# Kernel tuning notes

Hardware: AMD Instinct MI355X
Metric: run time of the kernel (lower is better)

Reference implementation:

```python
import jax, jax.numpy as jnp
import numpy as np

N_NODES = 100000
N_EDGES = 1600000
IN_F = 512
OUT_F = 128


def setup_inputs() -> dict:
    key = jax.random.key(0)
    k1, k2, k3, k4, k5 = jax.random.split(key, 5)
    x = jax.random.normal(k1, (N_NODES, IN_F), dtype=jnp.float32)
    adj_row = jnp.sort(jax.random.randint(k2, (N_EDGES,), 0, N_NODES, dtype=jnp.int32))
    adj_col = jax.random.randint(k3, (N_EDGES,), 0, N_NODES, dtype=jnp.int32)
    adj_vals = jax.random.uniform(k4, (N_EDGES,), dtype=jnp.float32)
    # Xavier-uniform init like nn.init.xavier_uniform_
    limit = float(np.sqrt(6.0 / (IN_F + OUT_F)))
    weight = jax.random.uniform(k5, (IN_F, OUT_F), minval=-limit, maxval=limit, dtype=jnp.float32)
    return {"x": x, "adj_row": adj_row, "adj_col": adj_col, "adj_vals": adj_vals, "weight": weight}


def reference(x, adj_row, adj_col, adj_vals, weight):
    # support = input @ weight  (dense GEMM; torch.spmm with dense-equivalent input)
    support = x @ weight                      # [N, OUT_F]
    # output = adj @ support, adj in COO: gather cols, scale, segment-sum by row
    msgs = adj_vals[:, None] * support[adj_col]          # [E, OUT_F]
    output = jax.ops.segment_sum(msgs, adj_row, num_segments=N_NODES)  # [N, OUT_F]
    return output
```

## Files before the change

### kernel.cpp

```cpp
#include <hip/hip_runtime.h>
#include <hip/hip_bf16.h>

typedef __bf16 bf16;
typedef __attribute__((ext_vector_type(8))) __bf16 bf16x8;
typedef __attribute__((ext_vector_type(4))) __bf16 bf16x4;
typedef __attribute__((ext_vector_type(2))) __bf16 bf16x2;
typedef __attribute__((ext_vector_type(4))) float f32x4;

#define IN_F 512
#define OUT_F 128
#define BM 64
#define BK 64
#define NKT (IN_F / BK)
#define CHUNK 128
#define UNR 16

__global__ __launch_bounds__(256) void wt_convert_kernel(const float* __restrict__ w,
                                                         bf16* __restrict__ wt) {
    int idx = blockIdx.x * 256 + threadIdx.x;
    int n = idx >> 9;
    int k = idx & 511;
    wt[idx] = (bf16)w[k * OUT_F + n];
}

__global__ __launch_bounds__(256) void gemm_kernel(const float* __restrict__ x,
                                                   const bf16* __restrict__ wt,
                                                   bf16* __restrict__ support,
                                                   int n_nodes) {
    __shared__ bf16 As[2][BM * BK];
    __shared__ bf16 Bs[2][OUT_F * BK];

    const int tid  = threadIdx.x;
    const int lane = tid & 63;
    const int wid  = tid >> 6;
    const int row0 = blockIdx.x * BM;

    float4 av[4];
    bf16x8 bv[4];

    auto load_tile = [&](int kt) {
        const int k0 = kt * BK;
        #pragma unroll
        for (int i = 0; i < 4; ++i) {
            int li = i * 256 + tid;
            int r = li >> 4, c4 = li & 15;
            int grow = row0 + r;
            float4 v = {0.f, 0.f, 0.f, 0.f};
            if (grow < n_nodes)
                v = *reinterpret_cast<const float4*>(x + (size_t)grow * IN_F + k0 + c4 * 4);
            av[i] = v;
        }
        #pragma unroll
        for (int i = 0; i < 4; ++i) {
            int li = i * 256 + tid;
            int r = li >> 3, c8 = li & 7;
            bv[i] = *reinterpret_cast<const bf16x8*>(wt + (size_t)r * IN_F + k0 + c8 * 8);
        }
    };

    auto write_tile = [&](int buf) {
        char* Ab = (char*)As[buf];
        char* Bb = (char*)Bs[buf];
        #pragma unroll
        for (int i = 0; i < 4; ++i) {
            int li = i * 256 + tid;
            int r = li >> 4, c4 = li & 15;
            bf16x4 b;
            b[0] = (bf16)av[i].x; b[1] = (bf16)av[i].y;
            b[2] = (bf16)av[i].z; b[3] = (bf16)av[i].w;
            *reinterpret_cast<bf16x4*>(Ab + ((r * 128 + c4 * 8) ^ ((r & 7) << 4))) = b;
        }
        #pragma unroll
        for (int i = 0; i < 4; ++i) {
            int li = i * 256 + tid;
            int r = li >> 3, c8 = li & 7;
            *reinterpret_cast<bf16x8*>(Bb + ((r * 128 + c8 * 16) ^ ((r & 7) << 4))) = bv[i];
        }
    };

    f32x4 acc[4][2] = {};

    load_tile(0);
    write_tile(0);
    __syncthreads();

    for (int kt = 0; kt < NKT; ++kt) {
        const int cur = kt & 1;
        if (kt < NKT - 1) load_tile(kt + 1);

        const char* Ab = (const char*)As[cur];
        const char* Bb = (const char*)Bs[cur];
        #pragma unroll
        for (int kk = 0; kk < 2; ++kk) {
            const int kbyte = kk * 64 + (lane >> 4) * 16;
            bf16x8 a[4], b[2];
            #pragma unroll
            for (int m = 0; m < 4; ++m) {
                int r = m * 16 + (lane & 15);
                a[m] = *reinterpret_cast<const bf16x8*>(Ab + ((r * 128 + kbyte) ^ ((r & 7) << 4)));
            }
            #pragma unroll
            for (int n = 0; n < 2; ++n) {
                int r = wid * 32 + n * 16 + (lane & 15);
                b[n] = *reinterpret_cast<const bf16x8*>(Bb + ((r * 128 + kbyte) ^ ((r & 7) << 4)));
            }
            #pragma unroll
            for (int m = 0; m < 4; ++m)
                #pragma unroll
                for (int n = 0; n < 2; ++n)
                    acc[m][n] = __builtin_amdgcn_mfma_f32_16x16x32_bf16(a[m], b[n], acc[m][n], 0, 0, 0);
        }

        if (kt < NKT - 1) {
            write_tile(cur ^ 1);
            __syncthreads();
        }
    }

    #pragma unroll
    for (int m = 0; m < 4; ++m) {
        #pragma unroll
        for (int n = 0; n < 2; ++n) {
            #pragma unroll
            for (int j = 0; j < 4; ++j) {
                int gm = row0 + m * 16 + (lane >> 4) * 4 + j;
                int gn = wid * 32 + n * 16 + (lane & 15);
                if (gm < n_nodes)
                    support[(size_t)gm * OUT_F + gn] = (bf16)acc[m][n][j];
            }
        }
    }
}

__global__ __launch_bounds__(64) void scatter_kernel(const int* __restrict__ adj_row,
                                                     const int* __restrict__ adj_col,
                                                     const float* __restrict__ adj_vals,
                                                     const bf16* __restrict__ support,
                                                     float* __restrict__ out,
                                                     int n_edges) {
    __shared__ int   srow[CHUNK];
    __shared__ int   scol[CHUNK];
    __shared__ float sval[CHUNK];

    const int t  = threadIdx.x;
    const int e0 = blockIdx.x * CHUNK;
    const int nE = min(CHUNK, n_edges - e0);

    for (int i = t; i < CHUNK; i += 64) {
        if (i < nE) {
            srow[i] = adj_row[e0 + i];
            scol[i] = adj_col[e0 + i];
            sval[i] = adj_vals[e0 + i];
        } else {
            srow[i] = adj_row[e0 + nE - 1];
            scol[i] = 0;
            sval[i] = 0.f;
        }
    }
    __syncthreads();

    const int firstRow = srow[0];

    float accx = 0.f, accy = 0.f;
    int   cur = firstRow;

    for (int i0 = 0; i0 < CHUNK; i0 += UNR) {
        float mx[UNR], my[UNR];
        #pragma unroll
        for (int u = 0; u < UNR; ++u) {
            int   c = scol[i0 + u];
            float s = sval[i0 + u];
            bf16x2 v = *reinterpret_cast<const bf16x2*>(support + (size_t)c * OUT_F + t * 2);
            mx[u] = s * (float)v[0];
            my[u] = s * (float)v[1];
        }
        #pragma unroll
        for (int u = 0; u < UNR; ++u) {
            int r = srow[i0 + u];
            if (r != cur) {
                float* dst = out + (size_t)cur * OUT_F + t * 2;
                if (cur == firstRow) {
                    atomicAdd(dst, accx); atomicAdd(dst + 1, accy);
                } else {
                    dst[0] = accx; dst[1] = accy;
                }
                accx = 0.f; accy = 0.f;
                cur = r;
            }
            accx += mx[u]; accy += my[u];
        }
    }
    float* dst = out + (size_t)cur * OUT_F + t * 2;
    atomicAdd(dst, accx); atomicAdd(dst + 1, accy);
}

extern "C" void kernel_launch(void* const* d_in, const int* in_sizes, int n_in,
                              void* d_out, int out_size, void* d_ws, size_t ws_size,
                              hipStream_t stream) {
    const float* x        = (const float*)d_in[0];
    const int*   adj_row  = (const int*)d_in[1];
    const int*   adj_col  = (const int*)d_in[2];
    const float* adj_vals = (const float*)d_in[3];
    const float* weight   = (const float*)d_in[4];
    float*       out      = (float*)d_out;

    const int n_nodes = in_sizes[0] / IN_F;
    const int n_edges = in_sizes[1];

    bf16* support = (bf16*)d_ws;
    bf16* wt      = (bf16*)((char*)d_ws + (size_t)n_nodes * OUT_F * 2);

    hipMemsetAsync(d_out, 0, (size_t)out_size * sizeof(float), stream);

    wt_convert_kernel<<<(IN_F * OUT_F) / 256, 256, 0, stream>>>(weight, wt);

    int gemm_blocks = (n_nodes + BM - 1) / BM;
    gemm_kernel<<<gemm_blocks, 256, 0, stream>>>(x, wt, support, n_nodes);

    int scat_blocks = (n_edges + CHUNK - 1) / CHUNK;
    scatter_kernel<<<scat_blocks, 64, 0, stream>>>(adj_row, adj_col, adj_vals,
                                                   support, out, n_edges);
}
```

Baseline: 129.7 us.

## Pre-swizzle weight into MFMA fragments and fuse output zeroing into GEMM

```diff
diff --git a/kernel.cpp b/kernel.cpp
--- a/kernel.cpp
+++ b/kernel.cpp
@@ -16,19 +16,23 @@
 #define UNR 16
 
 __global__ __launch_bounds__(256) void wt_convert_kernel(const float* __restrict__ w,
-                                                         bf16* __restrict__ wt) {
-    int idx = blockIdx.x * 256 + threadIdx.x;
-    int n = idx >> 9;
-    int k = idx & 511;
-    wt[idx] = (bf16)w[k * OUT_F + n];
+                                                         bf16* __restrict__ wt_frag) {
+    int o = blockIdx.x * 256 + threadIdx.x;
+    int e   = o & 7;
+    int l   = (o >> 3) & 63;
+    int nb  = (o >> 9) & 7;
+    int kkt = o >> 12;
+    int n = nb * 16 + (l & 15);
+    int k = (kkt >> 1) * 64 + (kkt & 1) * 32 + (l >> 4) * 8 + e;
+    wt_frag[o] = (bf16)w[k * OUT_F + n];
 }
 
 __global__ __launch_bounds__(256) void gemm_kernel(const float* __restrict__ x,
-                                                   const bf16* __restrict__ wt,
+                                                   const bf16* __restrict__ wt_frag,
                                                    bf16* __restrict__ support,
+                                                   float* __restrict__ out,
                                                    int n_nodes) {
     __shared__ bf16 As[2][BM * BK];
-    __shared__ bf16 Bs[2][OUT_F * BK];
 
     const int tid  = threadIdx.x;
     const int lane = tid & 63;
@@ -36,7 +40,6 @@
     const int row0 = blockIdx.x * BM;
 
     float4 av[4];
-    bf16x8 bv[4];
 
     auto load_tile = [&](int kt) {
         const int k0 = kt * BK;
@@ -50,17 +53,10 @@
                 v = *reinterpret_cast<const float4*>(x + (size_t)grow * IN_F + k0 + c4 * 4);
             av[i] = v;
         }
-        #pragma unroll
-        for (int i = 0; i < 4; ++i) {
-            int li = i * 256 + tid;
-            int r = li >> 3, c8 = li & 7;
-            bv[i] = *reinterpret_cast<const bf16x8*>(wt + (size_t)r * IN_F + k0 + c8 * 8);
-        }
     };
 
     auto write_tile = [&](int buf) {
         char* Ab = (char*)As[buf];
-        char* Bb = (char*)Bs[buf];
         #pragma unroll
         for (int i = 0; i < 4; ++i) {
             int li = i * 256 + tid;
@@ -70,45 +66,55 @@
             b[2] = (bf16)av[i].z; b[3] = (bf16)av[i].w;
             *reinterpret_cast<bf16x4*>(Ab + ((r * 128 + c4 * 8) ^ ((r & 7) << 4))) = b;
         }
-        #pragma unroll
-        for (int i = 0; i < 4; ++i) {
-            int li = i * 256 + tid;
-            int r = li >> 3, c8 = li & 7;
-            *reinterpret_cast<bf16x8*>(Bb + ((r * 128 + c8 * 16) ^ ((r & 7) << 4))) = bv[i];
-        }
     };
 
-    f32x4 acc[4][2] = {};
-
     load_tile(0);
+
+    {
+        float4 z = {0.f, 0.f, 0.f, 0.f};
+        const size_t lim = (size_t)n_nodes * OUT_F;
+        #pragma unroll
+        for (int i = 0; i < 8; ++i) {
+            size_t off = (size_t)row0 * OUT_F + (size_t)(i * 256 + tid) * 4;
+            if (off < lim)
+                *reinterpret_cast<float4*>(out + off) = z;
+        }
+    }
+
     write_tile(0);
     __syncthreads();
 
+    f32x4 acc[4][2] = {};
+
     for (int kt = 0; kt < NKT; ++kt) {
         const int cur = kt & 1;
+
+        bf16x8 b[2][2];
+        #pragma unroll
+        for (int kk = 0; kk < 2; ++kk)
+            #pragma unroll
+            for (int n = 0; n < 2; ++n) {
+                int f = (kt * 2 + kk) * 8 + (wid * 2 + n);
+                b[kk][n] = *reinterpret_cast<const bf16x8*>(wt_frag + ((size_t)f * 64 + lane) * 8);
+            }
+
         if (kt < NKT - 1) load_tile(kt + 1);
 
         const char* Ab = (const char*)As[cur];
-        const char* Bb = (const char*)Bs[cur];
         #pragma unroll
         for (int kk = 0; kk < 2; ++kk) {
             const int kbyte = kk * 64 + (lane >> 4) * 16;
-            bf16x8 a[4], b[2];
+            bf16x8 a[4];
             #pragma unroll
             for (int m = 0; m < 4; ++m) {
                 int r = m * 16 + (lane & 15);
                 a[m] = *reinterpret_cast<const bf16x8*>(Ab + ((r * 128 + kbyte) ^ ((r & 7) << 4)));
             }
             #pragma unroll
-            for (int n = 0; n < 2; ++n) {
-                int r = wid * 32 + n * 16 + (lane & 15);
-                b[n] = *reinterpret_cast<const bf16x8*>(Bb + ((r * 128 + kbyte) ^ ((r & 7) << 4)));
-            }
-            #pragma unroll
             for (int m = 0; m < 4; ++m)
                 #pragma unroll
                 for (int n = 0; n < 2; ++n)
-                    acc[m][n] = __builtin_amdgcn_mfma_f32_16x16x32_bf16(a[m], b[n], acc[m][n], 0, 0, 0);
+                    acc[m][n] = __builtin_amdgcn_mfma_f32_16x16x32_bf16(a[m], b[kk][n], acc[m][n], 0, 0, 0);
         }
 
         if (kt < NKT - 1) {
@@ -208,14 +214,12 @@
     const int n_edges = in_sizes[1];
 
     bf16* support = (bf16*)d_ws;
-    bf16* wt      = (bf16*)((char*)d_ws + (size_t)n_nodes * OUT_F * 2);
-
-    hipMemsetAsync(d_out, 0, (size_t)out_size * sizeof(float), stream);
-
-    wt_convert_kernel<<<(IN_F * OUT_F) / 256, 256, 0, stream>>>(weight, wt);
+    bf16* wt_frag = (bf16*)((char*)d_ws + (size_t)n_nodes * OUT_F * 2);
+
+    wt_convert_kernel<<<(IN_F * OUT_F) / 256, 256, 0, stream>>>(weight, wt_frag);
 
     int gemm_blocks = (n_nodes + BM - 1) / BM;
-    gemm_kernel<<<gemm_blocks, 256, 0, stream>>>(x, wt, support, n_nodes);
+    gemm_kernel<<<gemm_blocks, 256, 0, stream>>>(x, wt_frag, support, out, n_nodes);
 
     int scat_blocks = (n_edges + CHUNK - 1) / CHUNK;
     scatter_kernel<<<scat_blocks, 64, 0, stream>>>(adj_row, adj_col, adj_vals,
```

New measurement: 126.3 us. 2.6% less time.
